# Optimization experiments

Hardware: AMD Instinct MI355X
Metric: run time of the kernel (lower is better)

## Reference

```python
import jax, jax.numpy as jnp
import numpy as np

HIDDEN = 512
NSTEPS = 100
IN_DIM = 3
OUT_DIM = 3
BATCH = 16384


def _gru_cell(x, h, w_ih, w_hh, b_ih, b_hh):
    # torch.nn.GRUCell math; w_ih: [3H, in], w_hh: [3H, H]
    gi = x @ w_ih.T + b_ih  # [B, 3H]
    gh = h @ w_hh.T + b_hh  # [B, 3H]
    i_r, i_z, i_n = jnp.split(gi, 3, axis=-1)
    h_r, h_z, h_n = jnp.split(gh, 3, axis=-1)
    r = jax.nn.sigmoid(i_r + h_r)
    zt = jax.nn.sigmoid(i_z + h_z)
    n = jnp.tanh(i_n + r * h_n)
    return (1.0 - zt) * n + zt * h


def setup_inputs() -> dict:
    key = jax.random.key(0)
    ks = jax.random.split(key, 12)
    k = 1.0 / np.sqrt(HIDDEN)
    u = lambda kk, shape: jax.random.uniform(kk, shape, jnp.float32, -k, k)
    return {
        "z": jax.random.normal(ks[0], (BATCH, 6), jnp.float32),
        "w_ih1": u(ks[1], (3 * HIDDEN, IN_DIM)),
        "w_hh1": u(ks[2], (3 * HIDDEN, HIDDEN)),
        "b_ih1": u(ks[3], (3 * HIDDEN,)),
        "b_hh1": u(ks[4], (3 * HIDDEN,)),
        "w_ih2": u(ks[5], (3 * HIDDEN, HIDDEN)),
        "w_hh2": u(ks[6], (3 * HIDDEN, HIDDEN)),
        "b_ih2": u(ks[7], (3 * HIDDEN,)),
        "b_hh2": u(ks[8], (3 * HIDDEN,)),
        "fc_w": u(ks[9], (OUT_DIM, HIDDEN)),
        "fc_b": u(ks[10], (OUT_DIM,)),
    }


def reference(z, w_ih1, w_hh1, b_ih1, b_hh1, w_ih2, w_hh2, b_ih2, b_hh2, fc_w, fc_b):
    nbatch = z.shape[0]
    x0 = z[:, 3:]  # [B, 3]
    h1 = jnp.zeros((nbatch, HIDDEN), z.dtype)
    h2 = jnp.zeros((nbatch, HIDDEN), z.dtype)

    def step(carry, _):
        x, h1, h2 = carry
        h1 = _gru_cell(x, h1, w_ih1, w_hh1, b_ih1, b_hh1)
        h2 = _gru_cell(h1, h2, w_ih2, w_hh2, b_ih2, b_hh2)
        x = x + 0.1 * jnp.tanh(h2 @ fc_w.T + fc_b)
        return (x, h1, h2), x

    _, xs = jax.lax.scan(step, (x0, h1, h2), None, length=NSTEPS - 1)
    seq = jnp.concatenate([x0[None], xs], axis=0)  # [T, B, 3]
    return jnp.transpose(seq, (1, 0, 2))  # [B, T, 3]
```

## Files before the change

### kernel.cpp

```cpp
#include <hip/hip_runtime.h>

typedef _Float16 f16;
typedef _Float16 f16x8 __attribute__((ext_vector_type(8)));
typedef float f32x16 __attribute__((ext_vector_type(16)));

#define HID   512
#define BT    32
#define NSTEP 100
#define WMAT  786432

__device__ __forceinline__ float sigmoid_f(float x) {
  return 1.0f / (1.0f + __expf(-x));
}
__device__ __forceinline__ float tanh_f(float x) {
  float e = __expf(2.0f * x);
  return 1.0f - 2.0f / (e + 1.0f);
}
__device__ __forceinline__ f32x16 mfma16(f16x8 a, f16x8 b, f32x16 c) {
  return __builtin_amdgcn_mfma_f32_32x32x16_f16(a, b, c, 0, 0, 0);
}
__device__ __forceinline__ f32x16 zero16() {
  f32x16 z;
#pragma unroll
  for (int i = 0; i < 16; ++i) z[i] = 0.f;
  return z;
}

__global__ void pack_weights(const float* __restrict__ W, f16* __restrict__ out) {
  int t = blockIdx.x * 256 + threadIdx.x;
  if (t >= 48 * 32 * 64) return;
  int lane = t & 63;
  int kt   = (t >> 6) & 31;
  int ct   = t >> 11;
  int gate = ct * 32 + (lane & 31);
  int k0   = kt * 16 + (lane >> 5) * 8;
  const float* src = W + gate * HID + k0;
  f16x8 v;
#pragma unroll
  for (int i = 0; i < 8; ++i) v[i] = (f16)src[i];
  *(f16x8*)(out + (size_t)t * 8) = v;
}

__global__ void pack_wih1(const float* __restrict__ W, f16* __restrict__ out) {
  int t = blockIdx.x * 256 + threadIdx.x;
  if (t >= 48 * 64) return;
  int lane = t & 63;
  int ct   = t >> 6;
  int gate = ct * 32 + (lane & 31);
  int k0   = (lane >> 5) * 8;
  f16x8 v;
#pragma unroll
  for (int i = 0; i < 8; ++i) {
    int k = k0 + i;
    v[i] = (k < 3) ? (f16)W[gate * 3 + k] : (f16)0;
  }
  *(f16x8*)(out + (size_t)t * 8) = v;
}

__global__ void pack_bias(const float* __restrict__ bi, const float* __restrict__ bh,
                          float* __restrict__ out) {
  int j = blockIdx.x * 256 + threadIdx.x;
  if (j < 1024)      out[j] = bi[j] + bh[j];
  else if (j < 1536) out[j] = bi[j];
  else if (j < 2048) out[j] = bh[j - 512];
}

__global__ __launch_bounds__(512, 2) void gru_fused(
    const float* __restrict__ z,
    const float* __restrict__ fc_w,
    const float* __restrict__ fc_b,
    const f16*  __restrict__ Wp,
    const f16*  __restrict__ Wx,
    const float* __restrict__ Bb,
    float* __restrict__ out)
{
  __shared__ f16   h1s[2 * BT * HID];
  __shared__ f16   h2s[2 * BT * HID];
  __shared__ f16   xs16[BT * 16];
  __shared__ float fcwT[3 * HID];
  __shared__ float xsf[BT * 4];

  const int tid  = threadIdx.x;
  const int lane = tid & 63;
  const int wv   = tid >> 6;
  const int b0   = blockIdx.x * BT;

  {
    f16x8 z8 = {0, 0, 0, 0, 0, 0, 0, 0};
    for (int i = tid; i < BT * HID / 8; i += 512) {
      ((f16x8*)h1s)[i] = z8;
      ((f16x8*)h2s)[i] = z8;
    }
    if (tid < BT * 2) ((f16x8*)xs16)[tid] = z8;
    if (tid < HID) {
      const int pos = ((tid & 31) << 4) + (tid >> 5);
      fcwT[pos]              = fc_w[tid];
      fcwT[512 + pos]        = fc_w[512 + tid];
      fcwT[1024 + pos]       = fc_w[1024 + tid];
    }
  }
  __syncthreads();
  if (tid < BT * 3) {
    const int rr = tid / 3, oo = tid - rr * 3;
    float v = z[(size_t)(b0 + rr) * 6 + 3 + oo];
    xsf[rr * 4 + oo] = v;
    xs16[rr * 16 + oo] = (f16)v;
    out[(size_t)(b0 + rr) * 300 + oo] = v;
  }
  __syncthreads();

  const int colid = lane & 31;
  const int khalf = lane >> 5;
  const int klo   = khalf << 4;
  const int patA  = (colid & 7) << 4;
  const int rbase = colid * 1024;
  const int jw    = wv << 6;

  const f16* W1  = Wp;
  const f16* Wi2 = Wp + WMAT;
  const f16* Wh2 = Wp + 2 * WMAT;

  const int j0 = jw + colid, j1 = jw + 32 + colid;
  const float b1r0 = Bb[j0],         b1r1 = Bb[j1];
  const float b1z0 = Bb[512 + j0],   b1z1 = Bb[512 + j1];
  const float b1ni0 = Bb[1024 + j0], b1ni1 = Bb[1024 + j1];
  const float b1nh0 = Bb[1536 + j0], b1nh1 = Bb[1536 + j1];
  const float b2r0 = Bb[2048 + j0],         b2r1 = Bb[2048 + j1];
  const float b2z0 = Bb[2048 + 512 + j0],   b2z1 = Bb[2048 + 512 + j1];
  const float b2ni0 = Bb[2048 + 1024 + j0], b2ni1 = Bb[2048 + 1024 + j1];
  const float b2nh0 = Bb[2048 + 1536 + j0], b2nh1 = Bb[2048 + 1536 + j1];

  const float fb0 = fc_b[0], fb1 = fc_b[1], fb2 = fc_b[2];
  const int xoff = colid * 32 + klo;

  int p = 0;
  for (int t = 1; t < NSTEP; ++t) {
    const int q = p ^ 1;
    const char* h1r = (const char*)h1s + (p << 15);
    char*       h1w = (char*)h1s + (q << 15);
    const char* h2r = (const char*)h2s + (p << 15);
    char*       h2w = (char*)h2s + (q << 15);

#pragma unroll
    for (int c = 0; c < 2; ++c) {
      const int jb = jw + (c << 5);
      const int ct = jb >> 5;
      f32x16 aR, aZ, aN, aNx;
      {
        f16x8 ax  = *(const f16x8*)((const char*)xs16 + xoff);
        f16x8 brx = *(const f16x8*)(Wx + (size_t)ct * 512 + lane * 8);
        f16x8 bzx = *(const f16x8*)(Wx + (size_t)(16 + ct) * 512 + lane * 8);
        f16x8 bnx = *(const f16x8*)(Wx + (size_t)(32 + ct) * 512 + lane * 8);
        f32x16 zz = zero16();
        aR  = mfma16(ax, brx, zz);
        aZ  = mfma16(ax, bzx, zz);
        aNx = mfma16(ax, bnx, zz);
        aN  = zz;
      }
      const f16* Br = W1 + (size_t)ct * 16384 + lane * 8;
      const f16* Bz = W1 + (size_t)(16 + ct) * 16384 + lane * 8;
      const f16* Bn = W1 + (size_t)(32 + ct) * 16384 + lane * 8;
#pragma unroll 2
      for (int kt = 0; kt < 32; ++kt) {
        const int koff = ((kt << 5) | klo) ^ patA;
        f16x8 a0 = *(const f16x8*)(h1r + rbase + koff);
        aR = mfma16(a0, *(const f16x8*)(Br + kt * 512), aR);
        aZ = mfma16(a0, *(const f16x8*)(Bz + kt * 512), aZ);
        aN = mfma16(a0, *(const f16x8*)(Bn + kt * 512), aN);
      }
      const float brc  = c ? b1r1 : b1r0;
      const float bzc  = c ? b1z1 : b1z0;
      const float bnic = c ? b1ni1 : b1ni0;
      const float bnhc = c ? b1nh1 : b1nh0;
      const int jx = 2 * (jb + colid);
#pragma unroll
      for (int qq = 0; qq < 16; ++qq) {
        const int row = (qq & 3) + ((qq >> 2) << 3) + (khalf << 2);
        const int off = row * 1024 + (jx ^ ((row & 7) << 4));
        float r  = sigmoid_f(aR[qq] + brc);
        float zt = sigmoid_f(aZ[qq] + bzc);
        float n  = tanh_f(aNx[qq] + bnic + r * (aN[qq] + bnhc));
        float hold = (float)*(const f16*)(h1r + off);
        *(f16*)(h1w + off) = (f16)((1.0f - zt) * n + zt * hold);
      }
    }
    __syncthreads();

#pragma unroll
    for (int c = 0; c < 2; ++c) {
      const int jb = jw + (c << 5);
      const int ct = jb >> 5;
      f32x16 aR = zero16(), aZ = zero16(), aI = zero16(), aH = zero16();
      const f16* Bir = Wi2 + (size_t)ct * 16384 + lane * 8;
      const f16* Biz = Wi2 + (size_t)(16 + ct) * 16384 + lane * 8;
      const f16* Bin = Wi2 + (size_t)(32 + ct) * 16384 + lane * 8;
      const f16* Bhr = Wh2 + (size_t)ct * 16384 + lane * 8;
      const f16* Bhz = Wh2 + (size_t)(16 + ct) * 16384 + lane * 8;
      const f16* Bhn = Wh2 + (size_t)(32 + ct) * 16384 + lane * 8;
#pragma unroll 2
      for (int kt = 0; kt < 32; ++kt) {
        const int koff = ((kt << 5) | klo) ^ patA;
        f16x8 a1 = *(const f16x8*)(h1w + rbase + koff);
        f16x8 a2 = *(const f16x8*)(h2r + rbase + koff);
        aR = mfma16(a1, *(const f16x8*)(Bir + kt * 512), aR);
        aR = mfma16(a2, *(const f16x8*)(Bhr + kt * 512), aR);
        aZ = mfma16(a1, *(const f16x8*)(Biz + kt * 512), aZ);
        aZ = mfma16(a2, *(const f16x8*)(Bhz + kt * 512), aZ);
        aI = mfma16(a1, *(const f16x8*)(Bin + kt * 512), aI);
        aH = mfma16(a2, *(const f16x8*)(Bhn + kt * 512), aH);
      }
      const float brc  = c ? b2r1 : b2r0;
      const float bzc  = c ? b2z1 : b2z0;
      const float bnic = c ? b2ni1 : b2ni0;
      const float bnhc = c ? b2nh1 : b2nh0;
      const int jx = 2 * (jb + colid);
#pragma unroll
      for (int qq = 0; qq < 16; ++qq) {
        const int row = (qq & 3) + ((qq >> 2) << 3) + (khalf << 2);
        const int off = row * 1024 + (jx ^ ((row & 7) << 4));
        float r  = sigmoid_f(aR[qq] + brc);
        float zt = sigmoid_f(aZ[qq] + bzc);
        float n  = tanh_f(aI[qq] + bnic + r * (aH[qq] + bnhc));
        float hold = (float)*(const f16*)(h2r + off);
        *(f16*)(h2w + off) = (f16)((1.0f - zt) * n + zt * hold);
      }
    }
    __syncthreads();

    {
      const int row = (wv << 2) + (lane >> 4);
      const int sl  = lane & 15;
      const char* hb = h2w + row * 1024;
      const int pat = (row & 7) << 4;
      float p0 = 0.f, p1 = 0.f, p2 = 0.f;
#pragma unroll
      for (int j = 0; j < 4; ++j) {
        f16x8 hv8 = *(const f16x8*)(hb + ((((sl << 2) + j) << 4) ^ pat));
#pragma unroll
        for (int i = 0; i < 8; ++i) {
          const float hf = (float)hv8[i];
          const int kk = (j << 3) + i;
          p0 = fmaf(hf, fcwT[(kk << 4) + sl], p0);
          p1 = fmaf(hf, fcwT[512 + (kk << 4) + sl], p1);
          p2 = fmaf(hf, fcwT[1024 + (kk << 4) + sl], p2);
        }
      }
#pragma unroll
      for (int m = 1; m < 16; m <<= 1) {
        p0 += __shfl_xor(p0, m, 64);
        p1 += __shfl_xor(p1, m, 64);
        p2 += __shfl_xor(p2, m, 64);
      }
      if (sl == 0) {
        float x0 = xsf[(row << 2) + 0] + 0.1f * tanh_f(p0 + fb0);
        float x1 = xsf[(row << 2) + 1] + 0.1f * tanh_f(p1 + fb1);
        float x2 = xsf[(row << 2) + 2] + 0.1f * tanh_f(p2 + fb2);
        xsf[(row << 2) + 0] = x0;  xs16[row * 16 + 0] = (f16)x0;
        xsf[(row << 2) + 1] = x1;  xs16[row * 16 + 1] = (f16)x1;
        xsf[(row << 2) + 2] = x2;  xs16[row * 16 + 2] = (f16)x2;
        float* op = out + (size_t)(b0 + row) * 300 + (size_t)t * 3;
        op[0] = x0; op[1] = x1; op[2] = x2;
      }
    }
    __syncthreads();
    p ^= 1;
  }
}

extern "C" void kernel_launch(void* const* d_in, const int* in_sizes, int n_in,
                              void* d_out, int out_size, void* d_ws, size_t ws_size,
                              hipStream_t stream) {
  const float* z     = (const float*)d_in[0];
  const float* w_ih1 = (const float*)d_in[1];
  const float* w_hh1 = (const float*)d_in[2];
  const float* b_ih1 = (const float*)d_in[3];
  const float* b_hh1 = (const float*)d_in[4];
  const float* w_ih2 = (const float*)d_in[5];
  const float* w_hh2 = (const float*)d_in[6];
  const float* b_ih2 = (const float*)d_in[7];
  const float* b_hh2 = (const float*)d_in[8];
  const float* fc_w  = (const float*)d_in[9];
  const float* fc_b  = (const float*)d_in[10];
  float* out = (float*)d_out;

  f16*   Wp = (f16*)d_ws;
  f16*   Wx = (f16*)((char*)d_ws + (size_t)3 * WMAT * 2);
  float* Bb = (float*)((char*)d_ws + (size_t)3 * WMAT * 2 + 48 * 512 * 2);

  const int nbatch = in_sizes[0] / 6;

  pack_weights<<<384, 256, 0, stream>>>(w_hh1, Wp);
  pack_weights<<<384, 256, 0, stream>>>(w_ih2, Wp + WMAT);
  pack_weights<<<384, 256, 0, stream>>>(w_hh2, Wp + 2 * WMAT);
  pack_wih1<<<12, 256, 0, stream>>>(w_ih1, Wx);
  pack_bias<<<8, 256, 0, stream>>>(b_ih1, b_hh1, Bb);
  pack_bias<<<8, 256, 0, stream>>>(b_ih2, b_hh2, Bb + 2048);

  gru_fused<<<nbatch / BT, 512, 0, stream>>>(z, fc_w, fc_b, Wp, Wx, Bb, out);
}
```

Measured before the change: 12.65 ms.

## Double block size to 1024 threads, one column tile per wavefront

```diff
diff --git a/kernel.cpp b/kernel.cpp
--- a/kernel.cpp
+++ b/kernel.cpp
@@ -65,7 +65,7 @@
   else if (j < 2048) out[j] = bh[j - 512];
 }
 
-__global__ __launch_bounds__(512, 2) void gru_fused(
+__global__ __launch_bounds__(1024, 4) void gru_fused(
     const float* __restrict__ z,
     const float* __restrict__ fc_w,
     const float* __restrict__ fc_b,
@@ -87,16 +87,16 @@
 
   {
     f16x8 z8 = {0, 0, 0, 0, 0, 0, 0, 0};
-    for (int i = tid; i < BT * HID / 8; i += 512) {
+    for (int i = tid; i < BT * HID / 8; i += 1024) {
       ((f16x8*)h1s)[i] = z8;
       ((f16x8*)h2s)[i] = z8;
     }
     if (tid < BT * 2) ((f16x8*)xs16)[tid] = z8;
     if (tid < HID) {
-      const int pos = ((tid & 31) << 4) + (tid >> 5);
-      fcwT[pos]              = fc_w[tid];
-      fcwT[512 + pos]        = fc_w[512 + tid];
-      fcwT[1024 + pos]       = fc_w[1024 + tid];
+      const int pos = ((tid & 15) << 5) + (tid >> 4);
+      fcwT[pos]        = fc_w[tid];
+      fcwT[512 + pos]  = fc_w[512 + tid];
+      fcwT[1024 + pos] = fc_w[1024 + tid];
     }
   }
   __syncthreads();
@@ -114,37 +114,32 @@
   const int klo   = khalf << 4;
   const int patA  = (colid & 7) << 4;
   const int rbase = colid * 1024;
-  const int jw    = wv << 6;
+  const int jw    = wv << 5;
+  const int ct    = wv;
 
   const f16* W1  = Wp;
   const f16* Wi2 = Wp + WMAT;
   const f16* Wh2 = Wp + 2 * WMAT;
 
-  const int j0 = jw + colid, j1 = jw + 32 + colid;
-  const float b1r0 = Bb[j0],         b1r1 = Bb[j1];
-  const float b1z0 = Bb[512 + j0],   b1z1 = Bb[512 + j1];
-  const float b1ni0 = Bb[1024 + j0], b1ni1 = Bb[1024 + j1];
-  const float b1nh0 = Bb[1536 + j0], b1nh1 = Bb[1536 + j1];
-  const float b2r0 = Bb[2048 + j0],         b2r1 = Bb[2048 + j1];
-  const float b2z0 = Bb[2048 + 512 + j0],   b2z1 = Bb[2048 + 512 + j1];
-  const float b2ni0 = Bb[2048 + 1024 + j0], b2ni1 = Bb[2048 + 1024 + j1];
-  const float b2nh0 = Bb[2048 + 1536 + j0], b2nh1 = Bb[2048 + 1536 + j1];
+  const int j0 = jw + colid;
+  const float b1r = Bb[j0],         b1z = Bb[512 + j0];
+  const float b1ni = Bb[1024 + j0], b1nh = Bb[1536 + j0];
+  const float b2r = Bb[2048 + j0],         b2z = Bb[2048 + 512 + j0];
+  const float b2ni = Bb[2048 + 1024 + j0], b2nh = Bb[2048 + 1536 + j0];
 
   const float fb0 = fc_b[0], fb1 = fc_b[1], fb2 = fc_b[2];
   const int xoff = colid * 32 + klo;
+  const int jx = 2 * j0;
 
   int p = 0;
   for (int t = 1; t < NSTEP; ++t) {
-    const int q = p ^ 1;
+    const int qb = p ^ 1;
     const char* h1r = (const char*)h1s + (p << 15);
-    char*       h1w = (char*)h1s + (q << 15);
+    char*       h1w = (char*)h1s + (qb << 15);
     const char* h2r = (const char*)h2s + (p << 15);
-    char*       h2w = (char*)h2s + (q << 15);
-
-#pragma unroll
-    for (int c = 0; c < 2; ++c) {
-      const int jb = jw + (c << 5);
-      const int ct = jb >> 5;
+    char*       h2w = (char*)h2s + (qb << 15);
+
+    {
       f32x16 aR, aZ, aN, aNx;
       {
         f16x8 ax  = *(const f16x8*)((const char*)xs16 + xoff);
@@ -168,28 +163,20 @@
         aZ = mfma16(a0, *(const f16x8*)(Bz + kt * 512), aZ);
         aN = mfma16(a0, *(const f16x8*)(Bn + kt * 512), aN);
       }
-      const float brc  = c ? b1r1 : b1r0;
-      const float bzc  = c ? b1z1 : b1z0;
-      const float bnic = c ? b1ni1 : b1ni0;
-      const float bnhc = c ? b1nh1 : b1nh0;
-      const int jx = 2 * (jb + colid);
 #pragma unroll
       for (int qq = 0; qq < 16; ++qq) {
         const int row = (qq & 3) + ((qq >> 2) << 3) + (khalf << 2);
         const int off = row * 1024 + (jx ^ ((row & 7) << 4));
-        float r  = sigmoid_f(aR[qq] + brc);
-        float zt = sigmoid_f(aZ[qq] + bzc);
-        float n  = tanh_f(aNx[qq] + bnic + r * (aN[qq] + bnhc));
+        float r  = sigmoid_f(aR[qq] + b1r);
+        float zt = sigmoid_f(aZ[qq] + b1z);
+        float n  = tanh_f(aNx[qq] + b1ni + r * (aN[qq] + b1nh));
         float hold = (float)*(const f16*)(h1r + off);
         *(f16*)(h1w + off) = (f16)((1.0f - zt) * n + zt * hold);
       }
     }
     __syncthreads();
 
-#pragma unroll
-    for (int c = 0; c < 2; ++c) {
-      const int jb = jw + (c << 5);
-      const int ct = jb >> 5;
+    {
       f32x16 aR = zero16(), aZ = zero16(), aI = zero16(), aH = zero16();
       const f16* Bir = Wi2 + (size_t)ct * 16384 + lane * 8;
       const f16* Biz = Wi2 + (size_t)(16 + ct) * 16384 + lane * 8;
@@ -209,18 +196,13 @@
         aI = mfma16(a1, *(const f16x8*)(Bin + kt * 512), aI);
         aH = mfma16(a2, *(const f16x8*)(Bhn + kt * 512), aH);
       }
-      const float brc  = c ? b2r1 : b2r0;
-      const float bzc  = c ? b2z1 : b2z0;
-      const float bnic = c ? b2ni1 : b2ni0;
-      const float bnhc = c ? b2nh1 : b2nh0;
-      const int jx = 2 * (jb + colid);
 #pragma unroll
       for (int qq = 0; qq < 16; ++qq) {
         const int row = (qq & 3) + ((qq >> 2) << 3) + (khalf << 2);
         const int off = row * 1024 + (jx ^ ((row & 7) << 4));
-        float r  = sigmoid_f(aR[qq] + brc);
-        float zt = sigmoid_f(aZ[qq] + bzc);
-        float n  = tanh_f(aI[qq] + bnic + r * (aH[qq] + bnhc));
+        float r  = sigmoid_f(aR[qq] + b2r);
+        float zt = sigmoid_f(aZ[qq] + b2z);
+        float n  = tanh_f(aI[qq] + b2ni + r * (aH[qq] + b2nh));
         float hold = (float)*(const f16*)(h2r + off);
         *(f16*)(h2w + off) = (f16)((1.0f - zt) * n + zt * hold);
       }
@@ -228,25 +210,26 @@
     __syncthreads();
 
     {
-      const int row = (wv << 2) + (lane >> 4);
-      const int sl  = lane & 15;
+      const int row = (wv << 1) + (lane >> 5);
+      const int sl  = lane & 31;
       const char* hb = h2w + row * 1024;
       const int pat = (row & 7) << 4;
+      f16x8 ha = *(const f16x8*)(hb + ((sl << 5) ^ pat));
+      f16x8 hb8 = *(const f16x8*)(hb + (((sl << 5) | 16) ^ pat));
       float p0 = 0.f, p1 = 0.f, p2 = 0.f;
 #pragma unroll
-      for (int j = 0; j < 4; ++j) {
-        f16x8 hv8 = *(const f16x8*)(hb + ((((sl << 2) + j) << 4) ^ pat));
-#pragma unroll
-        for (int i = 0; i < 8; ++i) {
-          const float hf = (float)hv8[i];
-          const int kk = (j << 3) + i;
-          p0 = fmaf(hf, fcwT[(kk << 4) + sl], p0);
-          p1 = fmaf(hf, fcwT[512 + (kk << 4) + sl], p1);
-          p2 = fmaf(hf, fcwT[1024 + (kk << 4) + sl], p2);
-        }
-      }
-#pragma unroll
-      for (int m = 1; m < 16; m <<= 1) {
+      for (int i = 0; i < 8; ++i) {
+        const float hfa = (float)ha[i];
+        const float hfb = (float)hb8[i];
+        p0 = fmaf(hfa, fcwT[(i << 5) + sl], p0);
+        p1 = fmaf(hfa, fcwT[512 + (i << 5) + sl], p1);
+        p2 = fmaf(hfa, fcwT[1024 + (i << 5) + sl], p2);
+        p0 = fmaf(hfb, fcwT[((i + 8) << 5) + sl], p0);
+        p1 = fmaf(hfb, fcwT[512 + ((i + 8) << 5) + sl], p1);
+        p2 = fmaf(hfb, fcwT[1024 + ((i + 8) << 5) + sl], p2);
+      }
+#pragma unroll
+      for (int m = 1; m < 32; m <<= 1) {
         p0 += __shfl_xor(p0, m, 64);
         p1 += __shfl_xor(p1, m, 64);
         p2 += __shfl_xor(p2, m, 64);
@@ -296,5 +279,5 @@
   pack_bias<<<8, 256, 0, stream>>>(b_ih1, b_hh1, Bb);
   pack_bias<<<8, 256, 0, stream>>>(b_ih2, b_hh2, Bb + 2048);
 
-  gru_fused<<<nbatch / BT, 512, 0, stream>>>(z, fc_w, fc_b, Wp, Wx, Bb, out);
-}
+  gru_fused<<<nbatch / BT, 1024, 0, stream>>>(z, fc_w, fc_b, Wp, Wx, Bb, out);
+}
```

Result: slower. 17.51 ms (+38.5%).
